# Optimization experiments

Hardware: AMD Instinct MI355X
Metric: run time of the kernel (lower is better)

Reference implementation:

```python
import jax, jax.numpy as jnp
import numpy as np

SCENE = (128, 128, 16)
NUM_HEADS, NUM_LEVELS, NUM_POINTS = 8, 3, 4
FEAT_SHAPES = ((64, 192), (32, 96), (16, 48))


def _layer_norm(x, g, b, eps=1e-5):
    m = jnp.mean(x, -1, keepdims=True)
    v = jnp.var(x, -1, keepdims=True)
    return (x - m) * jax.lax.rsqrt(v + eps) * g + b


def _bilinear_sample(img, loc):
    # img: [B,H,W,D]; loc in [0,1] coords: [B,N,2] (x,y) -> [B,N,D]
    # matches F.grid_sample(mode='bilinear', padding_mode='zeros', align_corners=False)
    B, H, W, D = img.shape
    x = loc[..., 0] * W - 0.5
    y = loc[..., 1] * H - 0.5
    x0 = jnp.floor(x)
    y0 = jnp.floor(y)
    wx = x - x0
    wy = y - y0
    x0i = x0.astype(jnp.int32)
    y0i = y0.astype(jnp.int32)
    bi = jnp.arange(B)[:, None]

    def tap(ix, iy, w):
        valid = (ix >= 0) & (ix < W) & (iy >= 0) & (iy < H)
        v = img[bi, jnp.clip(iy, 0, H - 1), jnp.clip(ix, 0, W - 1)]
        return v * (w * valid)[..., None]

    return (tap(x0i, y0i, (1 - wx) * (1 - wy)) + tap(x0i + 1, y0i, wx * (1 - wy))
            + tap(x0i, y0i + 1, (1 - wx) * wy) + tap(x0i + 1, y0i + 1, wx * wy))


def _msdeform_attn(query, query_pos, value, ref_pts, Wv, bv, Woff, boff, Wattn, battn, Wout, bout):
    # mmcv MultiScaleDeformableAttention (batch_first), dropout=identity at eval.
    B, Nq, C = query.shape
    Hh, L, P = NUM_HEADS, NUM_LEVELS, NUM_POINTS
    Dh = C // Hh
    identity = query
    q = query + query_pos
    v = (value @ Wv + bv).reshape(B, -1, Hh, Dh)  # [B,S,Hh,Dh]
    off = (q @ Woff + boff).reshape(B, Nq, Hh, L, P, 2)
    aw = jax.nn.softmax((q @ Wattn + battn).reshape(B, Nq, Hh, L * P), axis=-1)
    aw = aw.reshape(B, Nq, Hh, L, P)
    # offset normalizer is (W_l, H_l) per level
    norm = jnp.asarray([[w, h] for (h, w) in FEAT_SHAPES], dtype=q.dtype)  # [L,2]
    loc = ref_pts[:, :, None, None, None, :] + off / norm[None, None, None, :, None, :]
    starts = np.cumsum([0] + [h * w for (h, w) in FEAT_SHAPES])
    acc = jnp.zeros((B * Hh, Nq, Dh), q.dtype)
    for l, (h, w) in enumerate(FEAT_SHAPES):
        img = v[:, starts[l]:starts[l + 1]].reshape(B, h, w, Hh, Dh)
        img = img.transpose(0, 3, 1, 2, 4).reshape(B * Hh, h, w, Dh)
        loc_l = loc[:, :, :, l].transpose(0, 2, 1, 3, 4).reshape(B * Hh, Nq * P, 2)
        sampled = _bilinear_sample(img, loc_l).reshape(B * Hh, Nq, P, Dh)
        w_l = aw[:, :, :, l].transpose(0, 2, 1, 3).reshape(B * Hh, Nq, P)
        acc = acc + jnp.einsum('bnp,bnpd->bnd', w_l, sampled)
    out = acc.reshape(B, Hh, Nq, Dh).transpose(0, 2, 1, 3).reshape(B, Nq, C)
    return identity + out @ Wout + bout


def _forward(scene_embed, scene_pos, ref_pix, feat0, feat1, feat2,
             Wv, bv, Woff, boff, Wattn, battn, Wout, bout, ln_g, ln_b,
             vol_pts, fov_mask):
    bs, V, C = scene_embed.shape
    ncam = fov_mask.shape[1]
    X, Y, Z = SCENE
    # in-bounds voxel mask built by scatter of valid projected points
    keep = ((vol_pts[..., 0] >= 0) & (vol_pts[..., 0] < X)
            & (vol_pts[..., 1] >= 0) & (vol_pts[..., 1] < Y)
            & (vol_pts[..., 2] >= 0) & (vol_pts[..., 2] < Z))
    flat = vol_pts[..., 0] * (Y * Z) + vol_pts[..., 1] * Z + vol_pts[..., 2]
    safe = jnp.where(keep, flat, 0)
    bi = jnp.arange(bs)[:, None]
    pts_mask = (jnp.zeros((bs, V), jnp.int32).at[bi, safe].max(keep.astype(jnp.int32)) > 0)

    # flatten_multi_scale_feats: [B, C, H, W] -> concat over levels of [B, HW, C]
    value = jnp.concatenate(
        [f.reshape(f.shape[0], C, -1).transpose(0, 2, 1) for f in (feat0, feat1, feat2)], axis=1)

    # Padded-equivalent dense dispatch: deformable attention is per-query independent,
    # so running it on ALL voxels per camera and masking on scatter-back is exactly the
    # math of the original ragged gather -> attend -> scatter pipeline.
    S = value.shape[1]
    q = jnp.broadcast_to(scene_embed[:, None], (bs, ncam, V, C)).reshape(bs * ncam, V, C)
    qp = jnp.broadcast_to(scene_pos[:, None], (bs, ncam, V, C)).reshape(bs * ncam, V, C)
    val = jnp.broadcast_to(value[:, None], (bs, ncam, S, C)).reshape(bs * ncam, S, C)
    ref = ref_pix.reshape(bs * ncam, V, 2)
    attn_out = _msdeform_attn(q, qp, val, ref, Wv, bv, Woff, boff, Wattn, battn, Wout, bout)
    attn_out = _layer_norm(attn_out, ln_g, ln_b).reshape(bs, ncam, V, C)

    # scatter back; later cameras overwrite earlier ones (matches python loop order)
    pts_embed = jnp.zeros((bs, V, C), scene_embed.dtype)
    for cam in range(ncam):
        m = (pts_mask & fov_mask[:, cam])[..., None]
        pts_embed = jnp.where(m, attn_out[:, cam], pts_embed)

    x3d = scene_embed.transpose(0, 2, 1)  # nlc_to_nchw then flatten(2): [bs, C, V]
    proposal = jnp.where(pts_mask[:, None, :], pts_embed.transpose(0, 2, 1), x3d)
    return proposal.reshape(bs, C, X, Y, Z)


def setup_inputs():
    key = jax.random.key(0)
    ks = jax.random.split(key, 16)
    C = 128
    X, Y, Z = SCENE
    V = X * Y * Z
    bs, ncam = 1, 1
    f32 = jnp.float32
    Hh, L, P = NUM_HEADS, NUM_LEVELS, NUM_POINTS
    s = 0.02
    vx = jax.random.randint(ks[2], (bs, V), -8, X + 8)
    vy = jax.random.randint(ks[3], (bs, V), -8, Y + 8)
    vz = jax.random.randint(ks[4], (bs, V), -2, Z + 2)
    return {
        'scene_embed': jax.random.normal(ks[0], (bs, V, C), f32),
        'scene_pos': jax.random.normal(ks[1], (bs, V, C), f32),
        'ref_pix': jax.random.uniform(ks[5], (bs, ncam, V, 2), dtype=f32),
        'feat0': jax.random.normal(ks[6], (bs * ncam, C, 64, 192), f32),
        'feat1': jax.random.normal(ks[7], (bs * ncam, C, 32, 96), f32),
        'feat2': jax.random.normal(ks[8], (bs * ncam, C, 16, 48), f32),
        'Wv': jax.random.normal(ks[9], (C, C), f32) * s,
        'bv': jnp.zeros((C,), f32),
        'Woff': jax.random.normal(ks[10], (C, Hh * L * P * 2), f32) * s,
        'boff': jax.random.normal(ks[11], (Hh * L * P * 2,), f32) * s,
        'Wattn': jax.random.normal(ks[12], (C, Hh * L * P), f32) * s,
        'battn': jnp.zeros((Hh * L * P,), f32),
        'Wout': jax.random.normal(ks[13], (C, C), f32) * s,
        'bout': jnp.zeros((C,), f32),
        'ln_g': jnp.ones((C,), f32),
        'ln_b': jnp.zeros((C,), f32),
        'vol_pts': jnp.stack([vx, vy, vz], -1).astype(jnp.int32),
        'fov_mask': jax.random.bernoulli(ks[14], 0.6, (bs, ncam, V)),
    }


def reference(scene_embed, scene_pos, ref_pix, feat0, feat1, feat2,
              Wv, bv, Woff, boff, Wattn, battn, Wout, bout, ln_g, ln_b,
              vol_pts, fov_mask):
    return _forward(scene_embed, scene_pos, ref_pix, feat0, feat1, feat2,
                    Wv, bv, Woff, boff, Wattn, battn, Wout, bout, ln_g, ln_b,
                    vol_pts, fov_mask)
```

## Files before the change

### kernel.cpp

```cpp
#include <hip/hip_runtime.h>


typedef __attribute__((ext_vector_type(8))) short short8v;
typedef __attribute__((ext_vector_type(8))) unsigned short u16x8;
typedef __attribute__((ext_vector_type(4))) float f32x4;

#define V_TOT 262144
#define OAS 292
#define NBLK_ATTN 2048

__device__ __forceinline__ unsigned short f2bf(float f) {
  unsigned int u = __float_as_uint(f);
  u += 0x7fffu + ((u >> 16) & 1u);
  return (unsigned short)(u >> 16);
}
__device__ __forceinline__ float bf2f(unsigned short h) {
  return __uint_as_float(((unsigned int)h) << 16);
}

__global__ void zero_kernel(unsigned int* pm) {
  pm[blockIdx.x * 512 + threadIdx.x] = 0u;
}

__global__ void scatter_kernel(const int* __restrict__ vp, unsigned char* __restrict__ pm) {
  int v = blockIdx.x * 512 + threadIdx.x;
  int x = vp[v * 3 + 0], y = vp[v * 3 + 1], z = vp[v * 3 + 2];
  if (x >= 0 && x < 128 && y >= 0 && y < 128 && z >= 0 && z < 16)
    pm[x * 2048 + y * 16 + z] = 1;
}

__global__ void probe_kernel(const unsigned char* __restrict__ fov, int* __restrict__ pflags) {
  int l = threadIdx.x;
  int n = l & 15, kb = (l >> 4) * 8;
  short8v a, b0, b17;
  #pragma unroll
  for (int e = 0; e < 8; ++e) {
    a[e]   = (short)f2bf((float)n);
    b0[e]  = (kb + e == 0)  ? (short)f2bf((float)(n + 1)) : (short)0;
    b17[e] = (kb + e == 17) ? (short)f2bf((float)(n + 3)) : (short)0;
  }
  f32x4 z = {0.f, 0.f, 0.f, 0.f};
  f32x4 d0  = __builtin_amdgcn_mfma_f32_16x16x32_bf16(a, b0,  z, 0, 0, 0);
  f32x4 d17 = __builtin_amdgcn_mfma_f32_16x16x32_bf16(a, b17, z, 0, 0, 0);
  bool ok0 = true, ok1 = true;
  #pragma unroll
  for (int r = 0; r < 4; ++r) {
    float rA = (float)((l >> 4) * 4 + r);
    float cA = (float)(l & 15);
    ok0 = ok0 && (d0[r] == rA * (cA + 1.f)) && (d17[r] == rA * (cA + 3.f));
    ok1 = ok1 && (d0[r] == cA * (rA + 1.f)) && (d17[r] == cA * (rA + 3.f));
  }
  bool all0 = __all(ok0), all1 = __all(ok1);
  if (l == 0) {
    pflags[0] = all0 ? 0 : (all1 ? 1 : 2);
    const unsigned int* fw = (const unsigned int*)fov;
    int i32mode = 1;
    for (int i = 0; i < 8; ++i) i32mode &= (fw[i] <= 1u) ? 1 : 0;
    pflags[1] = i32mode;
  }
}

__global__ void vproj_kernel(const float* __restrict__ f0, const float* __restrict__ f1,
                             const float* __restrict__ f2, const float* __restrict__ Wv,
                             const float* __restrict__ bv, unsigned short* __restrict__ vp) {
  __shared__ __align__(16) float lds[128][20];
  int t = threadIdx.x;
  int s0 = blockIdx.x * 16;
  const float* f; int hw, sl0;
  if (s0 < 12288)      { f = f0; hw = 12288; sl0 = s0; }
  else if (s0 < 15360) { f = f1; hw = 3072;  sl0 = s0 - 12288; }
  else                 { f = f2; hw = 768;   sl0 = s0 - 15360; }
  for (int u = 0; u < 8; ++u) {
    int idx = u * 256 + t;
    int k = idx >> 4, si = idx & 15;
    lds[k][si] = f[(size_t)k * hw + sl0 + si];
  }
  __syncthreads();
  {
    int c = t & 127, half = t >> 7;
    int base = half * 8;
    f32x4 acc0 = {0.f,0.f,0.f,0.f}, acc1 = {0.f,0.f,0.f,0.f};
    #pragma unroll 4
    for (int k = 0; k < 128; ++k) {
      float w = Wv[k * 128 + c];
      f32x4 l0 = *(const f32x4*)&lds[k][base];
      f32x4 l1 = *(const f32x4*)&lds[k][base + 4];
      acc0 += l0 * w;
      acc1 += l1 * w;
    }
    float b = bv[c];
    #pragma unroll
    for (int j = 0; j < 4; ++j) {
      vp[(size_t)(s0 + base + j)     * 128 + c] = f2bf(acc0[j] + b);
      vp[(size_t)(s0 + base + 4 + j) * 128 + c] = f2bf(acc1[j] + b);
    }
  }
}

__global__ void wfrag_kernel(const float* __restrict__ Woff, const float* __restrict__ Wattn,
                             const float* __restrict__ Wout,
                             unsigned short* __restrict__ foa_hi, unsigned short* __restrict__ foa_lo,
                             unsigned short* __restrict__ fout_hi, unsigned short* __restrict__ fout_lo) {
  int t = blockIdx.x * 512 + threadIdx.x;
  int e = t & 7, lane = (t >> 3) & 63, kc = (t >> 9) & 3, nt = t >> 11;
  int k = kc * 32 + (lane >> 4) * 8 + e;
  int j = nt * 16 + (lane & 15);
  float v = (j < 192) ? Woff[k * 192 + j] : ((j < 288) ? Wattn[k * 96 + (j - 192)] : 0.f);
  unsigned short hi = f2bf(v);
  foa_hi[t] = hi;
  foa_lo[t] = f2bf(v - bf2f(hi));
  if (t < 16384) {
    float w = Wout[k * 128 + j];
    unsigned short whi = f2bf(w);
    fout_hi[t] = whi;
    fout_lo[t] = f2bf(w - bf2f(whi));
  }
}

__global__ __launch_bounds__(256) void flagsA_kernel(
    const unsigned char* __restrict__ pmask, const unsigned char* __restrict__ fovmask,
    const int* __restrict__ pflags, unsigned char* __restrict__ flags8,
    unsigned int* __restrict__ blkcnt) {
  __shared__ unsigned int wc[4];
  __shared__ int s_fovint;
  int t = threadIdx.x, b = blockIdx.x;
  int lane = t & 63, wid = t >> 6;
  if (t == 0) s_fovint = pflags[1];
  __syncthreads();
  int v = b * 256 + t;
  int pm = pmask[v];
  int fv = s_fovint ? ((const int*)fovmask)[v] : (int)fovmask[v];
  int fl = pm ? (fv ? 2 : 1) : 0;
  flags8[v] = (unsigned char)fl;
  unsigned long long msk = __ballot(fl == 2);
  if (lane == 0) wc[wid] = (unsigned int)__popcll(msk);
  __syncthreads();
  if (t == 0) blkcnt[b] = wc[0] + wc[1] + wc[2] + wc[3];
}

__global__ __launch_bounds__(1024) void scan_kernel(
    const unsigned int* __restrict__ blkcnt, unsigned int* __restrict__ blkoff,
    unsigned int* __restrict__ counter) {
  __shared__ unsigned int s[1024];
  int t = threadIdx.x;
  unsigned int x = blkcnt[t];
  s[t] = x;
  __syncthreads();
  for (int off = 1; off < 1024; off <<= 1) {
    unsigned int y = (t >= off) ? s[t - off] : 0u;
    __syncthreads();
    s[t] += y;
    __syncthreads();
  }
  blkoff[t] = s[t] - x;
  if (t == 1023) *counter = s[1023];
}

__global__ __launch_bounds__(256) void flagsB_kernel(
    const unsigned char* __restrict__ flags8, const unsigned int* __restrict__ blkoff,
    int* __restrict__ act, int* __restrict__ pidx) {
  __shared__ unsigned int wc[4], wo[4];
  int t = threadIdx.x, b = blockIdx.x;
  int lane = t & 63, wid = t >> 6;
  int v = b * 256 + t;
  int fl = flags8[v];
  unsigned long long msk = __ballot(fl == 2);
  if (lane == 0) wc[wid] = (unsigned int)__popcll(msk);
  __syncthreads();
  if (t == 0) {
    unsigned int s = 0;
    #pragma unroll
    for (int w = 0; w < 4; ++w) { wo[w] = s; s += wc[w]; }
  }
  __syncthreads();
  if (fl == 2) {
    int pos = (int)(blkoff[b] + wo[wid]) + __popcll(msk & ((1ull << lane) - 1ull));
    act[pos] = v;
    pidx[v] = pos;
  }
}

__global__ __launch_bounds__(256) void writer_kernel(
    const float* __restrict__ embed, const unsigned char* __restrict__ flags8,
    const int* __restrict__ pidx, const float* __restrict__ abuf, int mode_buf,
    float* __restrict__ out) {
  __shared__ float tr[64][133];
  __shared__ int sfl[64];
  __shared__ int spx[64];
  int t = threadIdx.x;
  int v0 = blockIdx.x * 64;
  if (t < 64) {
    int fl = flags8[v0 + t];
    sfl[t] = fl;
    spx[t] = (fl == 2) ? pidx[v0 + t] : -1;
  }
  __syncthreads();
  #pragma unroll
  for (int rep = 0; rep < 8; ++rep) {
    int idx = rep * 256 + t;
    int i = idx >> 5, c4 = idx & 31;
    int fl = sfl[i];
    float4 val = {0.f, 0.f, 0.f, 0.f};
    if (mode_buf && fl == 2)
      val = *(const float4*)&abuf[(size_t)spx[i] * 128 + c4 * 4];
    else if (fl == 0)
      val = *(const float4*)&embed[(size_t)(v0 + i) * 128 + c4 * 4];
    tr[i][c4 * 4 + 0] = val.x;
    tr[i][c4 * 4 + 1] = val.y;
    tr[i][c4 * 4 + 2] = val.z;
    tr[i][c4 * 4 + 3] = val.w;
  }
  __syncthreads();
  float4* out4 = (float4*)out;
  #pragma unroll
  for (int rep = 0; rep < 8; ++rep) {
    int task = rep * 256 + t;
    int c = task >> 4, g = task & 15;
    float4 o;
    o.x = tr[g * 4 + 0][c];
    o.y = tr[g * 4 + 1][c];
    o.z = tr[g * 4 + 2][c];
    o.w = tr[g * 4 + 3][c];
    out4[(size_t)c * (V_TOT / 4) + (v0 >> 2) + g] = o;
  }
}

__global__ __launch_bounds__(512) void attn_kernel(
    const float* __restrict__ embed, const float* __restrict__ pos,
    const float* __restrict__ refp, const unsigned short* __restrict__ vproj,
    const unsigned short* __restrict__ WfragOAh, const unsigned short* __restrict__ WfragOAl,
    const unsigned short* __restrict__ WfragOuth, const unsigned short* __restrict__ WfragOutl,
    const float* __restrict__ boff, const float* __restrict__ battn,
    const float* __restrict__ bout, const float* __restrict__ lng, const float* __restrict__ lnb,
    const int* __restrict__ act, const unsigned int* __restrict__ counter,
    const int* __restrict__ pflags, float* __restrict__ abuf, int dstmode,
    float* __restrict__ out) {
  __shared__ __align__(16) float s_oa[32 * OAS];
  __shared__ __align__(16) unsigned short s_qhi[32 * 128];
  __shared__ __align__(16) unsigned short s_qlo[32 * 128];
  __shared__ int s_vidx[32];
  __shared__ float s_reff[64];
  __shared__ float s_boff[192], s_battn[96], s_bout[128], s_lng[128], s_lnb[128];
  __shared__ int s_meta[3];

  int t = threadIdx.x;
  int wid = t >> 6, lane = t & 63;

  if (t == 0) {
    int cnt = (int)*counter;
    s_meta[0] = cnt;
    s_meta[1] = pflags[0];
    s_meta[2] = (cnt + 31) >> 5;
  }
  if (t < 192) s_boff[t]  = boff[t];
  if (t < 96)  s_battn[t] = battn[t];
  if (t < 128) { s_bout[t] = bout[t]; s_lng[t] = lng[t]; s_lnb[t] = lnb[t]; }
  __syncthreads();
  int count = s_meta[0], mflag = s_meta[1], ntiles = s_meta[2];

  for (int tile = blockIdx.x; tile < ntiles; tile += NBLK_ATTN) {
    int q0 = tile * 32;
    if (t < 32) s_vidx[t] = (q0 + t < count) ? act[q0 + t] : -1;
    if (t < 64) {
      int i = t >> 1, comp = t & 1;
      int idx = q0 + i;
      int vid = (idx < count) ? act[idx] : -1;
      s_reff[t] = (vid >= 0) ? refp[(size_t)vid * 2 + comp] : 0.f;
    }
    {
      #pragma unroll
      for (int r = 0; r < 2; ++r) {
        int fi = r * 512 + t;
        int i = fi >> 5, c4 = fi & 31;
        int idx = q0 + i;
        int vid = (idx < count) ? act[idx] : -1;
        ushort4 hk = {0,0,0,0}, lk = {0,0,0,0};
        if (vid >= 0) {
          float4 ev = *(const float4*)(embed + (size_t)vid * 128 + c4 * 4);
          float4 pv = *(const float4*)(pos   + (size_t)vid * 128 + c4 * 4);
          float q_0 = ev.x + pv.x, q_1 = ev.y + pv.y, q_2 = ev.z + pv.z, q_3 = ev.w + pv.w;
          hk.x = f2bf(q_0); lk.x = f2bf(q_0 - bf2f(hk.x));
          hk.y = f2bf(q_1); lk.y = f2bf(q_1 - bf2f(hk.y));
          hk.z = f2bf(q_2); lk.z = f2bf(q_2 - bf2f(hk.z));
          hk.w = f2bf(q_3); lk.w = f2bf(q_3 - bf2f(hk.w));
        }
        int c = c4 * 4;
        int idxl = i * 128 + (((c >> 3) ^ (i & 7)) << 3) + (c & 7);
        *(ushort4*)&s_qhi[idxl] = hk;
        *(ushort4*)&s_qlo[idxl] = lk;
      }
    }
    __syncthreads();

    {
      int mrow = (wid & 1) * 16;
      int ntb = (wid >> 1) * 5;
      f32x4 acc[5];
      #pragma unroll
      for (int r = 0; r < 5; ++r) acc[r] = (f32x4){0.f,0.f,0.f,0.f};
      int arow = mrow + (lane & 15);
      int asub = lane >> 4;
      #pragma unroll 1
      for (int kc = 0; kc < 4; ++kc) {
        int slot = kc * 4 + asub;
        int aidx = arow * 128 + ((slot ^ (arow & 7)) << 3);
        short8v ah = *(const short8v*)&s_qhi[aidx];
        short8v al = *(const short8v*)&s_qlo[aidx];
        #pragma unroll
        for (int r = 0; r < 5; ++r) {
          size_t bi = (size_t)(((ntb + r) * 4 + kc) * 64 + lane) * 8;
          short8v bh = *(const short8v*)&WfragOAh[bi];
          short8v bl = *(const short8v*)&WfragOAl[bi];
          acc[r] = __builtin_amdgcn_mfma_f32_16x16x32_bf16(ah, bh, acc[r], 0, 0, 0);
          acc[r] = __builtin_amdgcn_mfma_f32_16x16x32_bf16(al, bh, acc[r], 0, 0, 0);
          acc[r] = __builtin_amdgcn_mfma_f32_16x16x32_bf16(ah, bl, acc[r], 0, 0, 0);
        }
      }
      #pragma unroll
      for (int r = 0; r < 5; ++r) {
        #pragma unroll
        for (int e = 0; e < 4; ++e) {
          int rr = (mflag == 0) ? ((lane >> 4) * 4 + e) : (lane & 15);
          int cc = (mflag == 0) ? (lane & 15) : ((lane >> 4) * 4 + e);
          int col = (ntb + r) * 16 + cc;
          if (col < 288) s_oa[(mrow + rr) * OAS + col] = acc[r][e];
        }
      }
    }
    __syncthreads();

    if (t < 256) {
      int i = t >> 3, h = t & 7;
      float* p = &s_oa[i * OAS + 192 + h * 12];
      const float* bb = &s_battn[h * 12];
      float l[12];
      float m = -1e30f;
      #pragma unroll
      for (int j = 0; j < 12; ++j) { l[j] = p[j] + bb[j]; m = fmaxf(m, l[j]); }
      float sum = 0.f;
      #pragma unroll
      for (int j = 0; j < 12; ++j) { l[j] = __expf(l[j] - m); sum += l[j]; }
      float inv = 1.0f / sum;
      #pragma unroll
      for (int j = 0; j < 12; ++j) p[j] = l[j] * inv;
    }
    __syncthreads();

    {
      const float invWn[3] = {1.f/192.f, 1.f/96.f, 1.f/48.f};
      const float invHn[3] = {1.f/64.f, 1.f/32.f, 1.f/16.f};
      float st[6][3];
      #pragma unroll
      for (int u = 0; u < 6; ++u) {
        int task = u * 512 + t;
        int i = task / 96, s = task % 96;
        int h = s / 12, lp = s % 12, l = lp >> 2, p = lp & 3;
        int oidx = ((h * 3 + l) * 4 + p) * 2;
        float ox = s_oa[i * OAS + oidx] + s_boff[oidx];
        float oy = s_oa[i * OAS + oidx + 1] + s_boff[oidx + 1];
        float aw = s_oa[i * OAS + 192 + h * 12 + lp];
        st[u][0] = s_reff[i * 2] + ox * invWn[l];
        st[u][1] = s_reff[i * 2 + 1] + oy * invHn[l];
        st[u][2] = aw;
      }
      __syncthreads();
      #pragma unroll
      for (int u = 0; u < 6; ++u) {
        int task = u * 512 + t;
        int i = task / 96, s = task % 96;
        float* d = &s_oa[i * OAS + s * 3];
        d[0] = st[u][0]; d[1] = st[u][1]; d[2] = st[u][2];
      }
    }
    __syncthreads();

    {
      int i = t >> 4, h = (t & 15) >> 1, half = t & 1;
      int dh0 = half * 8;
      float acc[8];
      #pragma unroll
      for (int e = 0; e < 8; ++e) acc[e] = 0.f;
      if (s_vidx[i] >= 0) {
        #pragma unroll 2
        for (int lp = 0; lp < 12; ++lp) {
          const int Wl = (lp < 4) ? 192 : ((lp < 8) ? 96 : 48);
          const int Hl = (lp < 4) ? 64 : ((lp < 8) ? 32 : 16);
          const int Bl = (lp < 4) ? 0 : ((lp < 8) ? 12288 : 15360);
          const float* pd = &s_oa[i * OAS + (h * 12 + lp) * 3];
          float lx = pd[0], ly = pd[1], aw = pd[2];
          float x = lx * (float)Wl - 0.5f, y = ly * (float)Hl - 0.5f;
          float xf = floorf(x), yf = floorf(y);
          float wx = x - xf, wy = y - yf;
          int x0 = (int)xf, y0 = (int)yf;
          int x1 = x0 + 1, y1 = y0 + 1;
          int x0c = min(max(x0, 0), Wl - 1), x1c = min(max(x1, 0), Wl - 1);
          int y0c = min(max(y0, 0), Hl - 1), y1c = min(max(y1, 0), Hl - 1);
          float vx0 = (x0 >= 0 && x0 < Wl) ? 1.f : 0.f;
          float vx1 = (x1 >= 0 && x1 < Wl) ? 1.f : 0.f;
          float vy0 = (y0 >= 0 && y0 < Hl) ? 1.f : 0.f;
          float vy1 = (y1 >= 0 && y1 < Hl) ? 1.f : 0.f;
          const unsigned short* vb = vproj + (size_t)Bl * 128 + h * 16 + dh0;
          u16x8 t00 = *(const u16x8*)(vb + (size_t)(y0c * Wl + x0c) * 128);
          u16x8 t01 = *(const u16x8*)(vb + (size_t)(y0c * Wl + x1c) * 128);
          u16x8 t10 = *(const u16x8*)(vb + (size_t)(y1c * Wl + x0c) * 128);
          u16x8 t11 = *(const u16x8*)(vb + (size_t)(y1c * Wl + x1c) * 128);
          float w00 = (1.f - wx) * (1.f - wy) * vx0 * vy0;
          float w01 = wx * (1.f - wy) * vx1 * vy0;
          float w10 = (1.f - wx) * wy * vx0 * vy1;
          float w11 = wx * wy * vx1 * vy1;
          #pragma unroll
          for (int e = 0; e < 8; ++e) {
            float sv = w00 * bf2f(t00[e]) + w01 * bf2f(t01[e])
                     + w10 * bf2f(t10[e]) + w11 * bf2f(t11[e]);
            acc[e] += aw * sv;
          }
        }
      }
      int c = h * 16 + dh0;
      int idxl = i * 128 + (((c >> 3) ^ (i & 7)) << 3);
      short8v hk, lk;
      #pragma unroll
      for (int e = 0; e < 8; ++e) {
        unsigned short hi = f2bf(acc[e]);
        hk[e] = (short)hi;
        lk[e] = (short)f2bf(acc[e] - bf2f(hi));
      }
      *(short8v*)&s_qhi[idxl] = hk;
      *(short8v*)&s_qlo[idxl] = lk;
    }
    __syncthreads();

    {
      int mrow = (wid & 1) * 16;
      int nt0 = (wid >> 1) * 2;
      f32x4 acc2[2];
      #pragma unroll
      for (int r = 0; r < 2; ++r) acc2[r] = (f32x4){0.f,0.f,0.f,0.f};
      int arow = mrow + (lane & 15);
      int asub = lane >> 4;
      #pragma unroll 1
      for (int kc = 0; kc < 4; ++kc) {
        int slot = kc * 4 + asub;
        int aidx = arow * 128 + ((slot ^ (arow & 7)) << 3);
        short8v ah = *(const short8v*)&s_qhi[aidx];
        short8v al = *(const short8v*)&s_qlo[aidx];
        #pragma unroll
        for (int r = 0; r < 2; ++r) {
          size_t bi = (size_t)(((nt0 + r) * 4 + kc) * 64 + lane) * 8;
          short8v bh = *(const short8v*)&WfragOuth[bi];
          short8v bl = *(const short8v*)&WfragOutl[bi];
          acc2[r] = __builtin_amdgcn_mfma_f32_16x16x32_bf16(ah, bh, acc2[r], 0, 0, 0);
          acc2[r] = __builtin_amdgcn_mfma_f32_16x16x32_bf16(al, bh, acc2[r], 0, 0, 0);
          acc2[r] = __builtin_amdgcn_mfma_f32_16x16x32_bf16(ah, bl, acc2[r], 0, 0, 0);
        }
      }
      #pragma unroll
      for (int r = 0; r < 2; ++r) {
        #pragma unroll
        for (int e = 0; e < 4; ++e) {
          int rr = (mflag == 0) ? ((lane >> 4) * 4 + e) : (lane & 15);
          int cc = (mflag == 0) ? (lane & 15) : ((lane >> 4) * 4 + e);
          int row = mrow + rr;
          int col = (nt0 + r) * 16 + cc;
          int vid = s_vidx[row];
          float idv = (vid >= 0) ? embed[(size_t)vid * 128 + col] : 0.f;
          s_oa[row * OAS + col] = acc2[r][e] + idv + s_bout[col];
        }
      }
    }
    __syncthreads();

    {
      int i = t >> 4, j = t & 15;
      float* rowp = &s_oa[i * OAS];
      float4 a = *(float4*)&rowp[j * 8];
      float4 b = *(float4*)&rowp[j * 8 + 4];
      float vals[8] = {a.x, a.y, a.z, a.w, b.x, b.y, b.z, b.w};
      float sum = 0.f, sq = 0.f;
      #pragma unroll
      for (int e = 0; e < 8; ++e) { sum += vals[e]; sq += vals[e] * vals[e]; }
      #pragma unroll
      for (int m = 1; m < 16; m <<= 1) {
        sum += __shfl_xor(sum, m);
        sq  += __shfl_xor(sq, m);
      }
      float mean = sum * (1.f / 128.f);
      float var = sq * (1.f / 128.f) - mean * mean;
      float rs = rsqrtf(var + 1e-5f);
      #pragma unroll
      for (int e = 0; e < 8; ++e) {
        int c = j * 8 + e;
        rowp[c] = (vals[e] - mean) * rs * s_lng[c] + s_lnb[c];
      }
    }
    __syncthreads();

    if (dstmode) {
      #pragma unroll
      for (int rep = 0; rep < 2; ++rep) {
        int idx = rep * 512 + t;
        int i = idx >> 5, c4 = idx & 31;
        if (s_vidx[i] >= 0) {
          float4 o;
          o.x = s_oa[i * OAS + c4 * 4 + 0];
          o.y = s_oa[i * OAS + c4 * 4 + 1];
          o.z = s_oa[i * OAS + c4 * 4 + 2];
          o.w = s_oa[i * OAS + c4 * 4 + 3];
          *(float4*)&abuf[(size_t)(q0 + i) * 128 + c4 * 4] = o;
        }
      }
    } else {
      #pragma unroll
      for (int rep = 0; rep < 8; ++rep) {
        int idx = rep * 512 + t;
        int c = idx >> 5, i = idx & 31;
        int vid = s_vidx[i];
        if (vid >= 0) out[(size_t)c * V_TOT + vid] = s_oa[i * OAS + c];
      }
    }
    __syncthreads();
  }
}

extern "C" void kernel_launch(void* const* d_in, const int* in_sizes, int n_in,
                              void* d_out, int out_size, void* d_ws, size_t ws_size,
                              hipStream_t stream) {
  const float* embed = (const float*)d_in[0];
  const float* pos   = (const float*)d_in[1];
  const float* refp  = (const float*)d_in[2];
  const float* f0    = (const float*)d_in[3];
  const float* f1    = (const float*)d_in[4];
  const float* f2    = (const float*)d_in[5];
  const float* Wv    = (const float*)d_in[6];
  const float* bv    = (const float*)d_in[7];
  const float* Woff  = (const float*)d_in[8];
  const float* boff  = (const float*)d_in[9];
  const float* Wattn = (const float*)d_in[10];
  const float* battn = (const float*)d_in[11];
  const float* Wout  = (const float*)d_in[12];
  const float* bout  = (const float*)d_in[13];
  const float* lng   = (const float*)d_in[14];
  const float* lnb   = (const float*)d_in[15];
  const int*   volp  = (const int*)d_in[16];
  const unsigned char* fov = (const unsigned char*)d_in[17];
  float* out = (float*)d_out;

  char* ws = (char*)d_ws;
  unsigned short* vproj  = (unsigned short*)(ws + 0);
  unsigned char*  pmask  = (unsigned char*)(ws + 4128768);
  unsigned int*   counter= (unsigned int*)(ws + 4390912);
  int*            pflags = (int*)(ws + 4391040);
  unsigned short* foa_hi = (unsigned short*)(ws + 4391168);
  unsigned short* foa_lo = (unsigned short*)(ws + 4473088);
  unsigned short* fout_hi= (unsigned short*)(ws + 4555008);
  unsigned short* fout_lo= (unsigned short*)(ws + 4587776);
  int*            act    = (int*)(ws + 4833536);
  unsigned char*  flags8 = (unsigned char*)(ws + 5882112);
  int*            pidx   = (int*)(ws + 6144256);
  unsigned int*   blkcnt = (unsigned int*)(ws + 7192832);
  unsigned int*   blkoff = (unsigned int*)(ws + 7196928);
  float*          abuf   = (float*)(ws + 7201024);

  int use_buf = (ws_size >= (size_t)7201024 + (size_t)134217728) ? 1 : 0;

  zero_kernel<<<128, 512, 0, stream>>>((unsigned int*)pmask);
  scatter_kernel<<<512, 512, 0, stream>>>(volp, pmask);
  probe_kernel<<<1, 64, 0, stream>>>(fov, pflags);
  vproj_kernel<<<1008, 256, 0, stream>>>(f0, f1, f2, Wv, bv, vproj);
  wfrag_kernel<<<80, 512, 0, stream>>>(Woff, Wattn, Wout, foa_hi, foa_lo,
                                       fout_hi, fout_lo);
  flagsA_kernel<<<1024, 256, 0, stream>>>(pmask, fov, pflags, flags8, blkcnt);
  scan_kernel<<<1, 1024, 0, stream>>>(blkcnt, blkoff, counter);
  flagsB_kernel<<<1024, 256, 0, stream>>>(flags8, blkoff, act, pidx);

  if (use_buf) {
    attn_kernel<<<NBLK_ATTN, 512, 0, stream>>>(embed, pos, refp, vproj,
                                               foa_hi, foa_lo, fout_hi, fout_lo,
                                               boff, battn, bout, lng, lnb,
                                               act, counter, pflags, abuf, 1, out);
    writer_kernel<<<4096, 256, 0, stream>>>(embed, flags8, pidx, abuf, 1, out);
  } else {
    writer_kernel<<<4096, 256, 0, stream>>>(embed, flags8, pidx, abuf, 0, out);
    attn_kernel<<<NBLK_ATTN, 512, 0, stream>>>(embed, pos, refp, vproj,
                                               foa_hi, foa_lo, fout_hi, fout_lo,
                                               boff, battn, bout, lng, lnb,
                                               act, counter, pflags, abuf, 0, out);
  }
}
```

Baseline: 324.7 us.

## Double attention block size and split bilinear gather across four lanes per head

The attention kernel now launches 1024 threads per block instead of 512. The deformable sampling stage assigns four threads per (query, head), each gathering 4 channels instead of 8, which doubles the number of threads issuing gathers. The matrix-multiply and layer-norm stages stay on the original 8 waves or 512 threads and are guarded so the extra threads sit idle there. The goal is more memory-level parallelism in the gather stage. The cost is narrower loads, a larger register limit per block from the new launch bounds, and idle waves during the GEMM phases.

```diff
diff --git a/kernel.cpp b/kernel.cpp
--- a/kernel.cpp
+++ b/kernel.cpp
@@ -2,7 +2,6 @@
 
 
 typedef __attribute__((ext_vector_type(8))) short short8v;
-typedef __attribute__((ext_vector_type(8))) unsigned short u16x8;
 typedef __attribute__((ext_vector_type(4))) float f32x4;
 
 #define V_TOT 262144
@@ -225,7 +224,7 @@
   }
 }
 
-__global__ __launch_bounds__(512) void attn_kernel(
+__global__ __launch_bounds__(1024) void attn_kernel(
     const float* __restrict__ embed, const float* __restrict__ pos,
     const float* __restrict__ refp, const unsigned short* __restrict__ vproj,
     const unsigned short* __restrict__ WfragOAh, const unsigned short* __restrict__ WfragOAl,
@@ -268,31 +267,28 @@
       s_reff[t] = (vid >= 0) ? refp[(size_t)vid * 2 + comp] : 0.f;
     }
     {
-      #pragma unroll
-      for (int r = 0; r < 2; ++r) {
-        int fi = r * 512 + t;
-        int i = fi >> 5, c4 = fi & 31;
-        int idx = q0 + i;
-        int vid = (idx < count) ? act[idx] : -1;
-        ushort4 hk = {0,0,0,0}, lk = {0,0,0,0};
-        if (vid >= 0) {
-          float4 ev = *(const float4*)(embed + (size_t)vid * 128 + c4 * 4);
-          float4 pv = *(const float4*)(pos   + (size_t)vid * 128 + c4 * 4);
-          float q_0 = ev.x + pv.x, q_1 = ev.y + pv.y, q_2 = ev.z + pv.z, q_3 = ev.w + pv.w;
-          hk.x = f2bf(q_0); lk.x = f2bf(q_0 - bf2f(hk.x));
-          hk.y = f2bf(q_1); lk.y = f2bf(q_1 - bf2f(hk.y));
-          hk.z = f2bf(q_2); lk.z = f2bf(q_2 - bf2f(hk.z));
-          hk.w = f2bf(q_3); lk.w = f2bf(q_3 - bf2f(hk.w));
-        }
-        int c = c4 * 4;
-        int idxl = i * 128 + (((c >> 3) ^ (i & 7)) << 3) + (c & 7);
-        *(ushort4*)&s_qhi[idxl] = hk;
-        *(ushort4*)&s_qlo[idxl] = lk;
-      }
-    }
-    __syncthreads();
-
-    {
+      int fi = t;
+      int i = fi >> 5, c4 = fi & 31;
+      int idx = q0 + i;
+      int vid = (idx < count) ? act[idx] : -1;
+      ushort4 hk = {0,0,0,0}, lk = {0,0,0,0};
+      if (vid >= 0) {
+        float4 ev = *(const float4*)(embed + (size_t)vid * 128 + c4 * 4);
+        float4 pv = *(const float4*)(pos   + (size_t)vid * 128 + c4 * 4);
+        float q_0 = ev.x + pv.x, q_1 = ev.y + pv.y, q_2 = ev.z + pv.z, q_3 = ev.w + pv.w;
+        hk.x = f2bf(q_0); lk.x = f2bf(q_0 - bf2f(hk.x));
+        hk.y = f2bf(q_1); lk.y = f2bf(q_1 - bf2f(hk.y));
+        hk.z = f2bf(q_2); lk.z = f2bf(q_2 - bf2f(hk.z));
+        hk.w = f2bf(q_3); lk.w = f2bf(q_3 - bf2f(hk.w));
+      }
+      int c = c4 * 4;
+      int idxl = i * 128 + (((c >> 3) ^ (i & 7)) << 3) + (c & 7);
+      *(ushort4*)&s_qhi[idxl] = hk;
+      *(ushort4*)&s_qlo[idxl] = lk;
+    }
+    __syncthreads();
+
+    if (wid < 8) {
       int mrow = (wid & 1) * 16;
       int ntb = (wid >> 1) * 5;
       f32x4 acc[5];
@@ -349,10 +345,10 @@
     {
       const float invWn[3] = {1.f/192.f, 1.f/96.f, 1.f/48.f};
       const float invHn[3] = {1.f/64.f, 1.f/32.f, 1.f/16.f};
-      float st[6][3];
-      #pragma unroll
-      for (int u = 0; u < 6; ++u) {
-        int task = u * 512 + t;
+      float st[3][3];
+      #pragma unroll
+      for (int u = 0; u < 3; ++u) {
+        int task = u * 1024 + t;
         int i = task / 96, s = task % 96;
         int h = s / 12, lp = s % 12, l = lp >> 2, p = lp & 3;
         int oidx = ((h * 3 + l) * 4 + p) * 2;
@@ -365,8 +361,8 @@
       }
       __syncthreads();
       #pragma unroll
-      for (int u = 0; u < 6; ++u) {
-        int task = u * 512 + t;
+      for (int u = 0; u < 3; ++u) {
+        int task = u * 1024 + t;
         int i = task / 96, s = task % 96;
         float* d = &s_oa[i * OAS + s * 3];
         d[0] = st[u][0]; d[1] = st[u][1]; d[2] = st[u][2];
@@ -375,11 +371,11 @@
     __syncthreads();
 
     {
-      int i = t >> 4, h = (t & 15) >> 1, half = t & 1;
-      int dh0 = half * 8;
-      float acc[8];
-      #pragma unroll
-      for (int e = 0; e < 8; ++e) acc[e] = 0.f;
+      int i = t >> 5, h = (t >> 2) & 7, q4 = t & 3;
+      int dh0 = q4 * 4;
+      float acc[4];
+      #pragma unroll
+      for (int e = 0; e < 4; ++e) acc[e] = 0.f;
       if (s_vidx[i] >= 0) {
         #pragma unroll 2
         for (int lp = 0; lp < 12; ++lp) {
@@ -400,37 +396,43 @@
           float vy0 = (y0 >= 0 && y0 < Hl) ? 1.f : 0.f;
           float vy1 = (y1 >= 0 && y1 < Hl) ? 1.f : 0.f;
           const unsigned short* vb = vproj + (size_t)Bl * 128 + h * 16 + dh0;
-          u16x8 t00 = *(const u16x8*)(vb + (size_t)(y0c * Wl + x0c) * 128);
-          u16x8 t01 = *(const u16x8*)(vb + (size_t)(y0c * Wl + x1c) * 128);
-          u16x8 t10 = *(const u16x8*)(vb + (size_t)(y1c * Wl + x0c) * 128);
-          u16x8 t11 = *(const u16x8*)(vb + (size_t)(y1c * Wl + x1c) * 128);
+          ushort4 t00 = *(const ushort4*)(vb + (size_t)(y0c * Wl + x0c) * 128);
+          ushort4 t01 = *(const ushort4*)(vb + (size_t)(y0c * Wl + x1c) * 128);
+          ushort4 t10 = *(const ushort4*)(vb + (size_t)(y1c * Wl + x0c) * 128);
+          ushort4 t11 = *(const ushort4*)(vb + (size_t)(y1c * Wl + x1c) * 128);
           float w00 = (1.f - wx) * (1.f - wy) * vx0 * vy0;
           float w01 = wx * (1.f - wy) * vx1 * vy0;
           float w10 = (1.f - wx) * wy * vx0 * vy1;
           float w11 = wx * wy * vx1 * vy1;
+          const unsigned short* p00 = (const unsigned short*)&t00;
+          const unsigned short* p01 = (const unsigned short*)&t01;
+          const unsigned short* p10 = (const unsigned short*)&t10;
+          const unsigned short* p11 = (const unsigned short*)&t11;
           #pragma unroll
-          for (int e = 0; e < 8; ++e) {
-            float sv = w00 * bf2f(t00[e]) + w01 * bf2f(t01[e])
-                     + w10 * bf2f(t10[e]) + w11 * bf2f(t11[e]);
+          for (int e = 0; e < 4; ++e) {
+            float sv = w00 * bf2f(p00[e]) + w01 * bf2f(p01[e])
+                     + w10 * bf2f(p10[e]) + w11 * bf2f(p11[e]);
             acc[e] += aw * sv;
           }
         }
       }
       int c = h * 16 + dh0;
-      int idxl = i * 128 + (((c >> 3) ^ (i & 7)) << 3);
-      short8v hk, lk;
-      #pragma unroll
-      for (int e = 0; e < 8; ++e) {
+      int idxl = i * 128 + (((c >> 3) ^ (i & 7)) << 3) + (c & 7);
+      ushort4 hk, lk;
+      unsigned short* hp = (unsigned short*)&hk;
+      unsigned short* lp2 = (unsigned short*)&lk;
+      #pragma unroll
+      for (int e = 0; e < 4; ++e) {
         unsigned short hi = f2bf(acc[e]);
-        hk[e] = (short)hi;
-        lk[e] = (short)f2bf(acc[e] - bf2f(hi));
-      }
-      *(short8v*)&s_qhi[idxl] = hk;
-      *(short8v*)&s_qlo[idxl] = lk;
-    }
-    __syncthreads();
-
-    {
+        hp[e] = hi;
+        lp2[e] = f2bf(acc[e] - bf2f(hi));
+      }
+      *(ushort4*)&s_qhi[idxl] = hk;
+      *(ushort4*)&s_qlo[idxl] = lk;
+    }
+    __syncthreads();
+
+    if (wid < 8) {
       int mrow = (wid & 1) * 16;
       int nt0 = (wid >> 1) * 2;
       f32x4 acc2[2];
@@ -470,7 +472,7 @@
     }
     __syncthreads();
 
-    {
+    if (t < 512) {
       int i = t >> 4, j = t & 15;
       float* rowp = &s_oa[i * OAS];
       float4 a = *(float4*)&rowp[j * 8];
@@ -496,23 +498,19 @@
     __syncthreads();
 
     if (dstmode) {
-      #pragma unroll
-      for (int rep = 0; rep < 2; ++rep) {
-        int idx = rep * 512 + t;
-        int i = idx >> 5, c4 = idx & 31;
-        if (s_vidx[i] >= 0) {
-          float4 o;
-          o.x = s_oa[i * OAS + c4 * 4 + 0];
-          o.y = s_oa[i * OAS + c4 * 4 + 1];
-          o.z = s_oa[i * OAS + c4 * 4 + 2];
-          o.w = s_oa[i * OAS + c4 * 4 + 3];
-          *(float4*)&abuf[(size_t)(q0 + i) * 128 + c4 * 4] = o;
-        }
+      int i = t >> 5, c4 = t & 31;
+      if (s_vidx[i] >= 0) {
+        float4 o;
+        o.x = s_oa[i * OAS + c4 * 4 + 0];
+        o.y = s_oa[i * OAS + c4 * 4 + 1];
+        o.z = s_oa[i * OAS + c4 * 4 + 2];
+        o.w = s_oa[i * OAS + c4 * 4 + 3];
+        *(float4*)&abuf[(size_t)(q0 + i) * 128 + c4 * 4] = o;
       }
     } else {
       #pragma unroll
-      for (int rep = 0; rep < 8; ++rep) {
-        int idx = rep * 512 + t;
+      for (int rep = 0; rep < 4; ++rep) {
+        int idx = rep * 1024 + t;
         int c = idx >> 5, i = idx & 31;
         int vid = s_vidx[i];
         if (vid >= 0) out[(size_t)c * V_TOT + vid] = s_oa[i * OAS + c];
@@ -574,16 +572,16 @@
   flagsB_kernel<<<1024, 256, 0, stream>>>(flags8, blkoff, act, pidx);
 
   if (use_buf) {
-    attn_kernel<<<NBLK_ATTN, 512, 0, stream>>>(embed, pos, refp, vproj,
-                                               foa_hi, foa_lo, fout_hi, fout_lo,
-                                               boff, battn, bout, lng, lnb,
-                                               act, counter, pflags, abuf, 1, out);
+    attn_kernel<<<NBLK_ATTN, 1024, 0, stream>>>(embed, pos, refp, vproj,
+                                                foa_hi, foa_lo, fout_hi, fout_lo,
+                                                boff, battn, bout, lng, lnb,
+                                                act, counter, pflags, abuf, 1, out);
     writer_kernel<<<4096, 256, 0, stream>>>(embed, flags8, pidx, abuf, 1, out);
   } else {
     writer_kernel<<<4096, 256, 0, stream>>>(embed, flags8, pidx, abuf, 0, out);
-    attn_kernel<<<NBLK_ATTN, 512, 0, stream>>>(embed, pos, refp, vproj,
-                                               foa_hi, foa_lo, fout_hi, fout_lo,
-                                               boff, battn, bout, lng, lnb,
-                                               act, counter, pflags, abuf, 0, out);
-  }
-}
+    attn_kernel<<<NBLK_ATTN, 1024, 0, stream>>>(embed, pos, refp, vproj,
+                                                foa_hi, foa_lo, fout_hi, fout_lo,
+                                                boff, battn, bout, lng, lnb,
+                                                act, counter, pflags, abuf, 0, out);
+  }
+}
```

Measured after the change: 424.5 us. 1.31x slower.
